# Kernel tuning notes

Measured on AMD Instinct MI355X. Metric: run time of the kernel, lower is better.

The kernel has to match this reference:

```python
import jax, jax.numpy as jnp
import numpy as np


def cmul(a, b):
    # complex multiply on (..., 2) real/imag pairs
    ar, ai = a[..., 0], a[..., 1]
    br, bi = b[..., 0], b[..., 1]
    return jnp.stack([ar * br - ai * bi, ar * bi + ai * br], axis=-1)


def butterfly_apply(x, diag, subdiag, superdiag, k):
    # x: [B, n, 2]; tridiagonal-at-offset-k complex matrix applied to x.
    # diag: [n, 2]; subdiag/superdiag padded to [n, 2], first n-k entries used.
    n = x.shape[-2]
    out = cmul(diag, x)
    out = out.at[..., k:, :].add(cmul(subdiag[: n - k], x[..., : n - k, :]))
    out = out.at[..., : n - k, :].add(cmul(superdiag[: n - k], x[..., k:, :]))
    return out


def block_perm(x, logit, s):
    # Soft block permutation: within each contiguous block of size s,
    # mix identity with even-odd separation (prob p0), then mix each half
    # with its reversal (probs p1, p2). Acts identically on real & imag.
    B, n, _ = x.shape
    p = jax.nn.sigmoid(logit)
    y = x.reshape(B, n // s, s, 2)
    eo = jnp.concatenate([y[:, :, 0::2, :], y[:, :, 1::2, :]], axis=2)
    y = (1 - p[0]) * y + p[0] * eo
    h = s // 2
    first = (1 - p[1]) * y[:, :, :h, :] + p[1] * jnp.flip(y[:, :, :h, :], axis=2)
    second = (1 - p[2]) * y[:, :, h:, :] + p[2] * jnp.flip(y[:, :, h:, :], axis=2)
    return jnp.concatenate([first, second], axis=2).reshape(B, n, 2)


def trifat_forward(x, perm_logits, diags, subdiags, superdiags, bias):
    B, n = x.shape
    depth, m = diags.shape[0], diags.shape[1]
    perm_sizes = [n >> i for i in range(m - 1)][::-1]  # 4, 8, ..., n
    # real_to_complex: zero imaginary part
    xc = jnp.stack([x, jnp.zeros_like(x)], axis=-1)  # [B, n, 2]
    for d in range(depth):
        for j, s in enumerate(perm_sizes):
            xc = block_perm(xc, perm_logits[d, j], s)
        for i in range(m):
            k = n >> (i + 1)  # offsets n/2, n/4, ..., 1
            xc = butterfly_apply(xc, diags[d, i], subdiags[d, i], superdiags[d, i], k)
    return xc[..., 0] + bias  # take real part, add bias


def setup_inputs() -> dict:
    key = jax.random.key(0)
    ks = jax.random.split(key, 6)
    B, n, depth = 4096, 1024, 2
    m = int(np.log2(n))
    return {
        "x": jax.random.normal(ks[0], (B, n), jnp.float32),
        "perm_logits": jax.random.normal(ks[1], (depth, m - 1, 3), jnp.float32),
        "diags": jax.random.normal(ks[2], (depth, m, n, 2), jnp.float32),
        "subdiags": jax.random.normal(ks[3], (depth, m, n, 2), jnp.float32),
        "superdiags": jax.random.normal(ks[4], (depth, m, n, 2), jnp.float32),
        "bias": jnp.zeros((n,), jnp.float32),
    }


def reference(x, perm_logits, diags, subdiags, superdiags, bias):
    return trifat_forward(x, perm_logits, diags, subdiags, superdiags, bias)
```

## Files before the change

kernel.cpp:

```cpp
#include <hip/hip_runtime.h>

#define N 1024
#define THREADS 256
#define EPT 4

__device__ __forceinline__ float2* run_pipeline(
    float2* bufA, float2* bufB, int tid,
    const float* __restrict__ logits,
    const float* __restrict__ diags,
    const float* __restrict__ subd,
    const float* __restrict__ supd)
{
    float2* src = bufA;
    float2* dst = bufB;

    for (int d = 0; d < 2; ++d) {
        for (int j = 0; j < 9; ++j) {
            const int s = 4 << j;
            const int h = s >> 1;
            const float* lg = logits + (d * 9 + j) * 3;
            const float p0 = 1.0f / (1.0f + expf(-lg[0]));
            const float p1 = 1.0f / (1.0f + expf(-lg[1]));
            const float p2 = 1.0f / (1.0f + expf(-lg[2]));
#pragma unroll
            for (int e = 0; e < EPT; ++e) {
                const int idx = tid + e * THREADS;
                const int base = idx & ~(s - 1);
                const int t = idx & (s - 1);
                const bool lo = (t < h);

                const int eo_t = lo ? (2 * t) : (2 * (t - h) + 1);
                const float2 xt  = src[idx];
                const float2 xeo = src[base + eo_t];
                float2 yt;
                yt.x = xt.x + p0 * (xeo.x - xt.x);
                yt.y = xt.y + p0 * (xeo.y - xt.y);

                const int tm = lo ? (h - 1 - t) : (s + h - 1 - t);
                const float psel = lo ? p1 : p2;
                const int eo_m = (tm < h) ? (2 * tm) : (2 * (tm - h) + 1);
                const float2 xm   = src[base + tm];
                const float2 xmeo = src[base + eo_m];
                float2 ym;
                ym.x = xm.x + p0 * (xmeo.x - xm.x);
                ym.y = xm.y + p0 * (xmeo.y - xm.y);

                float2 o;
                o.x = yt.x + psel * (ym.x - yt.x);
                o.y = yt.y + psel * (ym.y - yt.y);
                dst[idx] = o;
            }
            __syncthreads();
            float2* tmp = src; src = dst; dst = tmp;
        }
        for (int i = 0; i < 10; ++i) {
            const int k = N >> (i + 1);
            const float2* Dg = (const float2*)(diags + (size_t)((d * 10 + i) * N) * 2);
            const float2* Sb = (const float2*)(subd  + (size_t)((d * 10 + i) * N) * 2);
            const float2* Sp = (const float2*)(supd  + (size_t)((d * 10 + i) * N) * 2);
#pragma unroll
            for (int e = 0; e < EPT; ++e) {
                const int idx = tid + e * THREADS;
                const float2 xv = src[idx];
                const float2 dg = Dg[idx];
                float2 o;
                o.x = dg.x * xv.x - dg.y * xv.y;
                o.y = dg.x * xv.y + dg.y * xv.x;
                if (idx >= k) {
                    const float2 xs = src[idx - k];
                    const float2 sb = Sb[idx - k];
                    o.x += sb.x * xs.x - sb.y * xs.y;
                    o.y += sb.x * xs.y + sb.y * xs.x;
                }
                if (idx < N - k) {
                    const float2 xp = src[idx + k];
                    const float2 sp = Sp[idx];
                    o.x += sp.x * xp.x - sp.y * xp.y;
                    o.y += sp.x * xp.y + sp.y * xp.x;
                }
                dst[idx] = o;
            }
            __syncthreads();
            float2* tmp = src; src = dst; dst = tmp;
        }
    }
    return src;
}

__global__ __launch_bounds__(THREADS) void trifat_kernel(
    const float* __restrict__ x,
    const float* __restrict__ logits,
    const float* __restrict__ diags,
    const float* __restrict__ subd,
    const float* __restrict__ supd,
    const float* __restrict__ bias,
    float* __restrict__ out,
    int B)
{
    __shared__ float2 bufA[N];
    __shared__ float2 bufB[N];

    const int row = blockIdx.x;
    const int tid = threadIdx.x;
    if (row >= B) return;

    const float* xr = x + (size_t)row * N;
#pragma unroll
    for (int e = 0; e < EPT; ++e) {
        int idx = tid + e * THREADS;
        bufA[idx] = make_float2(xr[idx], 0.0f);
    }
    __syncthreads();

    float2* res = run_pipeline(bufA, bufB, tid, logits, diags, subd, supd);

    float* orow = out + (size_t)row * N;
#pragma unroll
    for (int e = 0; e < EPT; ++e) {
        int idx = tid + e * THREADS;
        orow[idx] = res[idx].x + bias[idx];
    }
}

__device__ __forceinline__ unsigned short f2bf_rne(float f) {
    unsigned int u = __float_as_uint(f);
    unsigned int r = u + 0x7fffu + ((u >> 16) & 1u);
    return (unsigned short)(r >> 16);
}

#define TBW 512
#define NB_BUILD 512

__global__ __launch_bounds__(TBW) void prep_kernel(
    const float* __restrict__ logits,
    const float* __restrict__ diags,
    const float* __restrict__ subd,
    const float* __restrict__ supd,
    const float* __restrict__ x,
    unsigned short* __restrict__ Bt,
    unsigned short* __restrict__ A2)
{
    __shared__ float2 buf[2][2][N];

    const int tid = threadIdx.x;

    if (blockIdx.x >= NB_BUILD) {
        const int cb = blockIdx.x - NB_BUILD;
        const size_t base4 = (size_t)cb * 4096;
#pragma unroll
        for (int r = 0; r < 8; ++r) {
            const size_t g4 = base4 + r * 512 + tid;
            const float4 v = *(const float4*)(x + g4 * 4);
            ushort4 o;
            o.x = f2bf_rne(v.x);
            o.y = f2bf_rne(v.y);
            o.z = f2bf_rne(v.z);
            o.w = f2bf_rne(v.w);
            *(ushort4*)(A2 + g4 * 4) = o;
        }
        return;
    }

    const int j0 = blockIdx.x * 2;

#pragma unroll
    for (int v = 0; v < 2; ++v)
#pragma unroll
        for (int e = 0; e < 2; ++e) {
            const int idx = tid + e * TBW;
            buf[0][v][idx] = make_float2(idx == (j0 + v) ? 1.0f : 0.0f, 0.0f);
        }
    __syncthreads();

    int sb = 0;
    for (int d = 0; d < 2; ++d) {
        for (int jp = 0; jp < 9; ++jp) {
            const int s = 4 << jp;
            const int h = s >> 1;
            const int hh = s >> 2;
            const float* lg = logits + (d * 9 + jp) * 3;
            const float p0 = 1.0f / (1.0f + expf(-lg[0]));
            const float p1 = 1.0f / (1.0f + expf(-lg[1]));
            const float p2 = 1.0f / (1.0f + expf(-lg[2]));
#pragma unroll
            for (int e = 0; e < 2; ++e) {
                const int tau = tid + e * TBW;
                const int v = tau >> 9;
                const int pid = tau & 511;
                const int w = pid & ((s >> 1) - 1);
                const int base = (pid >> (jp + 1)) << (jp + 2);

                int t, tm;
                float psel;
                if (w < hh) { t = w;          tm = h - 1 - w;  psel = p1; }
                else        { const int u = w - hh; t = h + u; tm = s - 1 - u; psel = p2; }

                const int eot = (t  < h) ? (2 * t)  : (2 * (t  - h) + 1);
                const int eom = (tm < h) ? (2 * tm) : (2 * (tm - h) + 1);

                const float2* src = buf[sb][v];
                float2* dst = buf[sb ^ 1][v];

                const float2 xt = src[base + t],  xet = src[base + eot];
                const float2 xm = src[base + tm], xem = src[base + eom];
                float2 yt, ym;
                yt.x = xt.x + p0 * (xet.x - xt.x);
                yt.y = xt.y + p0 * (xet.y - xt.y);
                ym.x = xm.x + p0 * (xem.x - xm.x);
                ym.y = xm.y + p0 * (xem.y - xm.y);

                float2 ot, om;
                ot.x = yt.x + psel * (ym.x - yt.x);
                ot.y = yt.y + psel * (ym.y - yt.y);
                om.x = ym.x + psel * (yt.x - ym.x);
                om.y = ym.y + psel * (yt.y - ym.y);
                dst[base + t]  = ot;
                dst[base + tm] = om;
            }
            __syncthreads();
            sb ^= 1;
        }
        for (int i = 0; i < 10; ++i) {
            const int k = N >> (i + 1);
            const float2* Dg  = (const float2*)(diags + (size_t)((d * 10 + i) * N) * 2);
            const float2* Sbc = (const float2*)(subd  + (size_t)((d * 10 + i) * N) * 2);
            const float2* Spc = (const float2*)(supd  + (size_t)((d * 10 + i) * N) * 2);
#pragma unroll
            for (int e = 0; e < 2; ++e) {
                const int idx = tid + e * TBW;
                const float2 dg = Dg[idx];
                float2 sbv = make_float2(0.f, 0.f), spv = make_float2(0.f, 0.f);
                if (idx >= k)     sbv = Sbc[idx - k];
                if (idx < N - k)  spv = Spc[idx];
#pragma unroll
                for (int v = 0; v < 2; ++v) {
                    const float2* src = buf[sb][v];
                    const float2 xv = src[idx];
                    float2 o;
                    o.x = dg.x * xv.x - dg.y * xv.y;
                    o.y = dg.x * xv.y + dg.y * xv.x;
                    if (idx >= k) {
                        const float2 xs = src[idx - k];
                        o.x += sbv.x * xs.x - sbv.y * xs.y;
                        o.y += sbv.x * xs.y + sbv.y * xs.x;
                    }
                    if (idx < N - k) {
                        const float2 xp = src[idx + k];
                        o.x += spv.x * xp.x - spv.y * xp.y;
                        o.y += spv.x * xp.y + spv.y * xp.x;
                    }
                    buf[sb ^ 1][v][idx] = o;
                }
            }
            __syncthreads();
            sb ^= 1;
        }
    }

#pragma unroll
    for (int v = 0; v < 2; ++v)
#pragma unroll
        for (int e = 0; e < 2; ++e) {
            const int idx = tid + e * TBW;
            Bt[(size_t)idx * N + (j0 + v)] = f2bf_rne(buf[sb][v][idx].x);
        }
}

typedef __attribute__((ext_vector_type(8))) __bf16 bf16x8;
typedef __attribute__((ext_vector_type(4))) float f32x4;

#define GLB(p) ((const __attribute__((address_space(1))) void*)(p))
#define LDS(p) ((__attribute__((address_space(3))) void*)(p))

__global__ __launch_bounds__(THREADS) void gemm_bf16(
    const unsigned short* __restrict__ A2,
    const unsigned short* __restrict__ Bt,
    const float* __restrict__ bias,
    float* __restrict__ out)
{
    __shared__ __align__(16) unsigned short As[64 * 64];
    __shared__ __align__(16) unsigned short Bs[64 * 64];

    const int m0 = blockIdx.x * 64;
    const int n0 = blockIdx.y * 64;
    const int tid = threadIdx.x;
    const int wave = tid >> 6, lane = tid & 63;
    const int wm = (wave >> 1) * 32, wn = (wave & 1) * 32;
    const int lrow = lane & 15, q = lane >> 4;
    const int r7 = lrow & 7;

    f32x4 acc[2][2] = {};

    for (int kt = 0; kt < 16; ++kt) {
        const int k0 = kt * 64;
        __syncthreads();
        {
            const unsigned short* gA = A2 + (size_t)m0 * N + k0;
            const unsigned short* gB = Bt + (size_t)n0 * N + k0;
#pragma unroll
            for (int r = 0; r < 2; ++r) {
                const int s = r * 256 + tid;
                const int row = s >> 3;
                const int gl = (s & 7) ^ (row & 7);
                __builtin_amdgcn_global_load_lds(GLB(gA + (size_t)row * N + gl * 8),
                                                 LDS(As + s * 8), 16, 0, 0);
                __builtin_amdgcn_global_load_lds(GLB(gB + (size_t)row * N + gl * 8),
                                                 LDS(Bs + s * 8), 16, 0, 0);
            }
        }
        __syncthreads();

#pragma unroll
        for (int kk = 0; kk < 64; kk += 32) {
            const int pg = ((kk >> 3) + q) ^ r7;
            bf16x8 a[2], b[2];
#pragma unroll
            for (int mi = 0; mi < 2; ++mi)
                a[mi] = *(const bf16x8*)(As + (wm + mi * 16 + lrow) * 64 + pg * 8);
#pragma unroll
            for (int ni = 0; ni < 2; ++ni)
                b[ni] = *(const bf16x8*)(Bs + (wn + ni * 16 + lrow) * 64 + pg * 8);
#pragma unroll
            for (int mi = 0; mi < 2; ++mi)
#pragma unroll
                for (int ni = 0; ni < 2; ++ni)
                    acc[mi][ni] = __builtin_amdgcn_mfma_f32_16x16x32_bf16(
                        a[mi], b[ni], acc[mi][ni], 0, 0, 0);
        }
    }

#pragma unroll
    for (int ni = 0; ni < 2; ++ni) {
        const int col = n0 + wn + ni * 16 + lrow;
        const float bv = bias[col];
#pragma unroll
        for (int mi = 0; mi < 2; ++mi)
#pragma unroll
            for (int r = 0; r < 4; ++r) {
                const int row = m0 + wm + mi * 16 + q * 4 + r;
                out[(size_t)row * N + col] = acc[mi][ni][r] + bv;
            }
    }
}

extern "C" void kernel_launch(void* const* d_in, const int* in_sizes, int n_in,
                              void* d_out, int out_size, void* d_ws, size_t ws_size,
                              hipStream_t stream) {
    const float* x      = (const float*)d_in[0];
    const float* logits = (const float*)d_in[1];
    const float* diags  = (const float*)d_in[2];
    const float* subd   = (const float*)d_in[3];
    const float* supd   = (const float*)d_in[4];
    const float* bias   = (const float*)d_in[5];
    float* out = (float*)d_out;

    const int B = in_sizes[0] / N;

    const size_t off_Bt = 0;
    const size_t off_A2 = 2u * 1024 * 1024;
    const size_t need   = off_A2 + (size_t)B * N * 2;

    if (ws_size >= need && B == 4096) {
        unsigned short* Bt = (unsigned short*)((char*)d_ws + off_Bt);
        unsigned short* A2 = (unsigned short*)((char*)d_ws + off_A2);

        prep_kernel<<<dim3(NB_BUILD + 256), dim3(TBW), 0, stream>>>(
            logits, diags, subd, supd, x, Bt, A2);
        gemm_bf16<<<dim3(B / 64, 16), dim3(THREADS), 0, stream>>>(A2, Bt, bias, out);
    } else {
        trifat_kernel<<<dim3(B), dim3(THREADS), 0, stream>>>(
            x, logits, diags, subd, supd, bias, out, B);
    }
}
```

Measured before the change: 135.7 us.

## Sparsify first-depth permutation and vectorize butterfly stages with prefetched coefficients

The prep kernel builds the dense transform matrix by pushing basis vectors through the pipeline. In the first depth pass, the permutation stages now process only the one block that holds the nonzero basis entry, since the other blocks are known to stay zero. Both buffers are zero-initialised to make this valid. Butterfly stages now handle two adjacent elements per thread with float4 LDS accesses. They also prefetch the next stage's diagonal coefficients during the current stage to hide global-load latency. The added control flow and register pressure are the tradeoff, and the speedup is limited to the prep portion of the total runtime.

```diff
diff --git a/kernel.cpp b/kernel.cpp
--- a/kernel.cpp
+++ b/kernel.cpp
@@ -140,7 +140,7 @@
     unsigned short* __restrict__ Bt,
     unsigned short* __restrict__ A2)
 {
-    __shared__ float2 buf[2][2][N];
+    __shared__ __align__(16) float2 buf[2][2][N];
 
     const int tid = threadIdx.x;
 
@@ -162,14 +162,17 @@
     }
 
     const int j0 = blockIdx.x * 2;
-
-#pragma unroll
-    for (int v = 0; v < 2; ++v)
-#pragma unroll
-        for (int e = 0; e < 2; ++e) {
-            const int idx = tid + e * TBW;
-            buf[0][v][idx] = make_float2(idx == (j0 + v) ? 1.0f : 0.0f, 0.0f);
-        }
+    const int t = tid;
+
+#pragma unroll
+    for (int b = 0; b < 2; ++b)
+#pragma unroll
+        for (int v = 0; v < 2; ++v)
+#pragma unroll
+            for (int e = 0; e < 2; ++e)
+                buf[b][v][tid + e * TBW] = make_float2(0.0f, 0.0f);
+    __syncthreads();
+    if (tid < 2) buf[0][tid][j0 + tid] = make_float2(1.0f, 0.0f);
     __syncthreads();
 
     int sb = 0;
@@ -182,75 +185,144 @@
             const float p0 = 1.0f / (1.0f + expf(-lg[0]));
             const float p1 = 1.0f / (1.0f + expf(-lg[1]));
             const float p2 = 1.0f / (1.0f + expf(-lg[2]));
-#pragma unroll
-            for (int e = 0; e < 2; ++e) {
-                const int tau = tid + e * TBW;
-                const int v = tau >> 9;
-                const int pid = tau & 511;
-                const int w = pid & ((s >> 1) - 1);
-                const int base = (pid >> (jp + 1)) << (jp + 2);
-
-                int t, tm;
+
+            int w = -1, base = 0;
+            if (d == 0) {
+                if (tid < (s >> 1)) {
+                    w = tid;
+                    base = (j0 >> (jp + 2)) << (jp + 2);
+                }
+            } else {
+                w = tid & ((s >> 1) - 1);
+                base = (tid >> (jp + 1)) << (jp + 2);
+            }
+
+            if (w >= 0) {
+                int tt, tm;
                 float psel;
-                if (w < hh) { t = w;          tm = h - 1 - w;  psel = p1; }
-                else        { const int u = w - hh; t = h + u; tm = s - 1 - u; psel = p2; }
-
-                const int eot = (t  < h) ? (2 * t)  : (2 * (t  - h) + 1);
+                if (w < hh) { tt = w;         tm = h - 1 - w;  psel = p1; }
+                else        { const int u = w - hh; tt = h + u; tm = s - 1 - u; psel = p2; }
+
+                const int eot = (tt < h) ? (2 * tt) : (2 * (tt - h) + 1);
                 const int eom = (tm < h) ? (2 * tm) : (2 * (tm - h) + 1);
 
-                const float2* src = buf[sb][v];
-                float2* dst = buf[sb ^ 1][v];
-
-                const float2 xt = src[base + t],  xet = src[base + eot];
-                const float2 xm = src[base + tm], xem = src[base + eom];
-                float2 yt, ym;
-                yt.x = xt.x + p0 * (xet.x - xt.x);
-                yt.y = xt.y + p0 * (xet.y - xt.y);
-                ym.x = xm.x + p0 * (xem.x - xm.x);
-                ym.y = xm.y + p0 * (xem.y - xm.y);
-
-                float2 ot, om;
-                ot.x = yt.x + psel * (ym.x - yt.x);
-                ot.y = yt.y + psel * (ym.y - yt.y);
-                om.x = ym.x + psel * (yt.x - ym.x);
-                om.y = ym.y + psel * (yt.y - ym.y);
-                dst[base + t]  = ot;
-                dst[base + tm] = om;
+#pragma unroll
+                for (int v = 0; v < 2; ++v) {
+                    const float2* src = buf[sb][v];
+                    float2* dst = buf[sb ^ 1][v];
+
+                    const float2 xt = src[base + tt], xet = src[base + eot];
+                    const float2 xm = src[base + tm], xem = src[base + eom];
+                    float2 yt, ym;
+                    yt.x = xt.x + p0 * (xet.x - xt.x);
+                    yt.y = xt.y + p0 * (xet.y - xt.y);
+                    ym.x = xm.x + p0 * (xem.x - xm.x);
+                    ym.y = xm.y + p0 * (xem.y - xm.y);
+
+                    float2 ot, om;
+                    ot.x = yt.x + psel * (ym.x - yt.x);
+                    ot.y = yt.y + psel * (ym.y - yt.y);
+                    om.x = ym.x + psel * (yt.x - ym.x);
+                    om.y = ym.y + psel * (yt.y - ym.y);
+                    dst[base + tt] = ot;
+                    dst[base + tm] = om;
+                }
             }
             __syncthreads();
             sb ^= 1;
         }
-        for (int i = 0; i < 10; ++i) {
+
+        float4 dg4, sb4, sp4;
+        {
+            const float4* Dg4 = (const float4*)(diags + (size_t)((d * 10) * N) * 2);
+            const float4* Sb4 = (const float4*)(subd  + (size_t)((d * 10) * N) * 2);
+            const float4* Sp4 = (const float4*)(supd  + (size_t)((d * 10) * N) * 2);
+            dg4 = Dg4[t];
+            sb4 = (t >= 256) ? Sb4[t - 256] : make_float4(0.f, 0.f, 0.f, 0.f);
+            sp4 = (t < 256)  ? Sp4[t]       : make_float4(0.f, 0.f, 0.f, 0.f);
+        }
+        for (int i = 0; i < 9; ++i) {
             const int k = N >> (i + 1);
-            const float2* Dg  = (const float2*)(diags + (size_t)((d * 10 + i) * N) * 2);
-            const float2* Sbc = (const float2*)(subd  + (size_t)((d * 10 + i) * N) * 2);
-            const float2* Spc = (const float2*)(supd  + (size_t)((d * 10 + i) * N) * 2);
-#pragma unroll
-            for (int e = 0; e < 2; ++e) {
-                const int idx = tid + e * TBW;
-                const float2 dg = Dg[idx];
-                float2 sbv = make_float2(0.f, 0.f), spv = make_float2(0.f, 0.f);
-                if (idx >= k)     sbv = Sbc[idx - k];
-                if (idx < N - k)  spv = Spc[idx];
-#pragma unroll
-                for (int v = 0; v < 2; ++v) {
-                    const float2* src = buf[sb][v];
-                    const float2 xv = src[idx];
-                    float2 o;
-                    o.x = dg.x * xv.x - dg.y * xv.y;
-                    o.y = dg.x * xv.y + dg.y * xv.x;
-                    if (idx >= k) {
-                        const float2 xs = src[idx - k];
-                        o.x += sbv.x * xs.x - sbv.y * xs.y;
-                        o.y += sbv.x * xs.y + sbv.y * xs.x;
-                    }
-                    if (idx < N - k) {
-                        const float2 xp = src[idx + k];
-                        o.x += spv.x * xp.x - spv.y * xp.y;
-                        o.y += spv.x * xp.y + spv.y * xp.x;
-                    }
-                    buf[sb ^ 1][v][idx] = o;
-                }
+            const int k2 = k >> 1;
+
+            float4 dg4n, sb4n, sp4n;
+            if (i < 8) {
+                const int kn2 = k2 >> 1;
+                const float4* Dg4 = (const float4*)(diags + (size_t)((d * 10 + i + 1) * N) * 2);
+                const float4* Sb4 = (const float4*)(subd  + (size_t)((d * 10 + i + 1) * N) * 2);
+                const float4* Sp4 = (const float4*)(supd  + (size_t)((d * 10 + i + 1) * N) * 2);
+                dg4n = Dg4[t];
+                sb4n = (t >= kn2)       ? Sb4[t - kn2] : make_float4(0.f, 0.f, 0.f, 0.f);
+                sp4n = (t < 512 - kn2)  ? Sp4[t]       : make_float4(0.f, 0.f, 0.f, 0.f);
+            }
+
+            const bool has_sb = (t >= k2);
+            const bool has_sp = (t < 512 - k2);
+#pragma unroll
+            for (int v = 0; v < 2; ++v) {
+                const float2* src = buf[sb][v];
+                const float4 xv = *(const float4*)(&src[2 * t]);
+                float4 o;
+                o.x = dg4.x * xv.x - dg4.y * xv.y;
+                o.y = dg4.x * xv.y + dg4.y * xv.x;
+                o.z = dg4.z * xv.z - dg4.w * xv.w;
+                o.w = dg4.z * xv.w + dg4.w * xv.z;
+                if (has_sb) {
+                    const float4 xs = *(const float4*)(&src[2 * t - k]);
+                    o.x += sb4.x * xs.x - sb4.y * xs.y;
+                    o.y += sb4.x * xs.y + sb4.y * xs.x;
+                    o.z += sb4.z * xs.z - sb4.w * xs.w;
+                    o.w += sb4.z * xs.w + sb4.w * xs.z;
+                }
+                if (has_sp) {
+                    const float4 xp = *(const float4*)(&src[2 * t + k]);
+                    o.x += sp4.x * xp.x - sp4.y * xp.y;
+                    o.y += sp4.x * xp.y + sp4.y * xp.x;
+                    o.z += sp4.z * xp.z - sp4.w * xp.w;
+                    o.w += sp4.z * xp.w + sp4.w * xp.z;
+                }
+                *(float4*)(&buf[sb ^ 1][v][2 * t]) = o;
+            }
+            __syncthreads();
+            sb ^= 1;
+            if (i < 8) { dg4 = dg4n; sb4 = sb4n; sp4 = sp4n; }
+        }
+        {
+            const float2* Dg = (const float2*)(diags + (size_t)((d * 10 + 9) * N) * 2);
+            const float2* Sb = (const float2*)(subd  + (size_t)((d * 10 + 9) * N) * 2);
+            const float2* Sp = (const float2*)(supd  + (size_t)((d * 10 + 9) * N) * 2);
+            const int i0 = 2 * t, i1 = 2 * t + 1;
+            const float2 dg0 = Dg[i0], dg1 = Dg[i1];
+            const float2 sb0 = (t >= 1) ? Sb[i0 - 1] : make_float2(0.f, 0.f);
+            const float2 sb1 = Sb[i0];
+            const float2 sp0 = Sp[i0];
+            const float2 sp1 = (t < 511) ? Sp[i1] : make_float2(0.f, 0.f);
+#pragma unroll
+            for (int v = 0; v < 2; ++v) {
+                const float2* src = buf[sb][v];
+                const float2 x0 = src[i0], x1 = src[i1];
+                float2 o0, o1;
+                o0.x = dg0.x * x0.x - dg0.y * x0.y;
+                o0.y = dg0.x * x0.y + dg0.y * x0.x;
+                o1.x = dg1.x * x1.x - dg1.y * x1.y;
+                o1.y = dg1.x * x1.y + dg1.y * x1.x;
+                if (t >= 1) {
+                    const float2 xs = src[i0 - 1];
+                    o0.x += sb0.x * xs.x - sb0.y * xs.y;
+                    o0.y += sb0.x * xs.y + sb0.y * xs.x;
+                }
+                o1.x += sb1.x * x0.x - sb1.y * x0.y;
+                o1.y += sb1.x * x0.y + sb1.y * x0.x;
+                o0.x += sp0.x * x1.x - sp0.y * x1.y;
+                o0.y += sp0.x * x1.y + sp0.y * x1.x;
+                if (t < 511) {
+                    const float2 xp = src[i1 + 1];
+                    o1.x += sp1.x * xp.x - sp1.y * xp.y;
+                    o1.y += sp1.x * xp.y + sp1.y * xp.x;
+                }
+                float4 ow;
+                ow.x = o0.x; ow.y = o0.y; ow.z = o1.x; ow.w = o1.y;
+                *(float4*)(&buf[sb ^ 1][v][i0]) = ow;
             }
             __syncthreads();
             sb ^= 1;
```

Result: faster. 125.0 us (-7.9%).
